# Optimization experiments

Measured on AMD Instinct MI355X. Metric: run time of the kernel, lower is better.

The kernel has to match this reference:

```python
import jax, jax.numpy as jnp
import numpy as np

B, L, D, H, P = 8, 1024, 128, 128, 8
W = 2 * L  # total words
FT = 0.1   # forget-gate floor


def _lin_init(k, out_d, in_d):
    k1, k2 = jax.random.split(k)
    s = 1.0 / np.sqrt(in_d)
    Wm = jax.random.uniform(k1, (out_d, in_d), minval=-s, maxval=s, dtype=jnp.float32)
    b = jax.random.uniform(k2, (out_d,), minval=-s, maxval=s, dtype=jnp.float32)
    return Wm, b


def setup_inputs() -> dict:
    key = jax.random.key(0)
    ks = jax.random.split(key, 32)
    inp = {
        "word_span0": jax.random.normal(ks[0], (B, L, D), dtype=jnp.float32),
        "word_span1": jax.random.normal(ks[1], (B, L, D), dtype=jnp.float32),
        "node_hidden": jax.random.normal(ks[2], (B, D), dtype=jnp.float32),
        "op_embedding": jax.random.normal(ks[3], (B, P, D), dtype=jnp.float32),
        "word_exist_sequence": jax.random.uniform(ks[4], (B, W), dtype=jnp.float32),
        "word_exist_matrix": jax.random.uniform(ks[5], (B, W, W), dtype=jnp.float32),
        "word_operator": jax.random.uniform(ks[6], (B, W, P), dtype=jnp.float32),
        "word_word": jax.random.uniform(ks[7], (B, W, W), dtype=jnp.float32),
        "depend0": jax.random.uniform(ks[8], (B, L, L), dtype=jnp.float32),
        "depend1": jax.random.uniform(ks[9], (B, L, L), dtype=jnp.float32),
        "goal_word": jax.random.uniform(ks[10], (B, W), dtype=jnp.float32),
    }
    dims = [("w_w_s", H, D), ("w_w_k", H, D), ("w_update", D, 3 * H),
            ("g_w", H, D), ("w_o", D, D), ("b2u_forget", D, 3 * H + D),
            ("b2u_forget2", D, 2 * D), ("linear_output", D, D),
            ("o_w", H, D), ("w_g", D, D), ("u2b_forget", D, 2 * D),
            ("w_o_forget", P, D + P * D), ("w_o_rel", P, D + P * D),
            ("w_o_update", P, 2 * P)]
    for i, (nm, o, ii) in enumerate(dims):
        Wm, b = _lin_init(ks[11 + i], o, ii)
        inp[nm + "_W"] = Wm
        inp[nm + "_b"] = b
    return inp


def _lin(x, Wm, b):
    return x @ Wm.T + b


def _nrm(m):
    # row-normalize by count of nonzero entries (torch normalize_matrix)
    return m / ((m != 0).sum(-1, keepdims=True).astype(m.dtype) + 1e-30)


def _l2(x):
    return x / (jnp.linalg.norm(x, axis=-1, keepdims=True) + 1e-30)


def _hgcn(span0, span1, node_hidden, op_emb, wes, wem, w_op, ww, dep0, dep1, gw, p):
    # ---- Bottom2Up ----
    all_word = jnp.concatenate([span0, span1], axis=1)              # [B,W,D]
    goal_trans = _lin(node_hidden, p["g_w_W"], p["g_w_b"])[:, None, :]  # [B,1,H]
    word_g = _l2(goal_trans * gw[..., None])                        # [B,W,H]
    wk_trans = _lin(all_word, p["w_w_k_W"], p["w_w_k_b"])           # [B,W,H]
    word_w_k = _l2(_nrm(ww * wem) @ wk_trans)                       # [B,W,H]
    word_w_s = _l2(jnp.concatenate(
        [_nrm(dep0) @ _lin(span0, p["w_w_s_W"], p["w_w_s_b"]),
         _nrm(dep1) @ _lin(span1, p["w_w_s_W"], p["w_w_s_b"])], axis=1))
    neighbor = jnp.concatenate([word_g, word_w_k, word_w_s], axis=-1)  # [B,W,3H]
    forget = jax.nn.sigmoid(_lin(jnp.concatenate([all_word, word_g, word_w_k, word_w_s], axis=-1),
                                 p["b2u_forget_W"], p["b2u_forget_b"]))
    word_updated = jnp.clip(forget, FT) * all_word + (1 - forget) * jax.nn.relu(
        _lin(neighbor, p["w_update_W"], p["w_update_b"]))           # [B,W,D]
    word_op = _nrm(jnp.swapaxes(wes[..., None] * w_op, 1, 2)) @ _lin(
        word_updated, p["w_o_W"], p["w_o_b"])                       # [B,P,D]
    forget2 = jax.nn.sigmoid(_lin(jnp.concatenate([op_emb, word_op], axis=-1),
                                  p["b2u_forget2_W"], p["b2u_forget2_b"]))
    op_emb = jnp.clip(forget2, FT) * op_emb + (1 - forget2) * jax.nn.relu(
        _lin(word_op, p["linear_output_W"], p["linear_output_b"]))  # [B,P,D]

    # ---- update_graph ----
    awe_n = _l2(word_updated)
    op_n = _l2(op_emb).reshape(op_emb.shape[0], -1)                 # [B,P*D]
    concate = jnp.concatenate(
        [awe_n, jnp.broadcast_to(op_n[:, None, :], (awe_n.shape[0], awe_n.shape[1], op_n.shape[-1]))],
        axis=-1)                                                    # [B,W,D+P*D]
    fg = jnp.clip(jax.nn.sigmoid(_lin(concate, p["w_o_forget_W"], p["w_o_forget_b"])), FT)
    upd = jax.nn.softmax(jax.nn.relu(_lin(
        jnp.concatenate([w_op, _lin(concate, p["w_o_rel_W"], p["w_o_rel_b"])], axis=-1),
        p["w_o_update_W"], p["w_o_update_b"])), axis=-1)
    w_op_new = fg * w_op + (1 - fg) * upd                           # [B,W,P]

    # ---- Up2Bottom ----
    span0u, span1u = word_updated[:, :L], word_updated[:, L:]
    word_o = _l2(w_op_new @ _lin(op_emb, p["o_w_W"], p["o_w_b"]))   # [B,W,H]
    word_w_k2 = _l2(_nrm(ww * wem) @ _lin(word_updated, p["w_w_k_W"], p["w_w_k_b"]))
    word_w_s2 = _l2(jnp.concatenate(
        [_nrm(dep0) @ _lin(span0u, p["w_w_s_W"], p["w_w_s_b"]),
         _nrm(dep1) @ _lin(span1u, p["w_w_s_W"], p["w_w_s_b"])], axis=1))
    neighbor2 = jnp.concatenate([word_o, word_w_k2, word_w_s2], axis=-1)
    word_updated2 = jax.nn.relu(_lin(neighbor2, p["w_update_W"], p["w_update_b"]))  # [B,W,D]
    goal_w = jnp.einsum('bw,bwd->bd', _nrm(gw * wes), word_updated2)  # [B,D]
    goal_updated = jax.nn.relu(_lin(goal_w, p["w_g_W"], p["w_g_b"]))
    fg3 = jax.nn.sigmoid(_lin(jnp.concatenate([goal_w, node_hidden], axis=-1),
                              p["u2b_forget_W"], p["u2b_forget_b"]))
    goal_next = jnp.clip(fg3, FT) * node_hidden + (1 - fg3) * goal_updated
    return (span0u, span1u, op_emb, goal_next)


def reference(word_span0, word_span1, node_hidden, op_embedding, word_exist_sequence,
              word_exist_matrix, word_operator, word_word, depend0, depend1, goal_word,
              w_w_s_W, w_w_s_b, w_w_k_W, w_w_k_b, w_update_W, w_update_b,
              g_w_W, g_w_b, w_o_W, w_o_b, b2u_forget_W, b2u_forget_b,
              b2u_forget2_W, b2u_forget2_b, linear_output_W, linear_output_b,
              o_w_W, o_w_b, w_g_W, w_g_b, u2b_forget_W, u2b_forget_b,
              w_o_forget_W, w_o_forget_b, w_o_rel_W, w_o_rel_b, w_o_update_W, w_o_update_b):
    p = dict(w_w_s_W=w_w_s_W, w_w_s_b=w_w_s_b, w_w_k_W=w_w_k_W, w_w_k_b=w_w_k_b,
             w_update_W=w_update_W, w_update_b=w_update_b, g_w_W=g_w_W, g_w_b=g_w_b,
             w_o_W=w_o_W, w_o_b=w_o_b, b2u_forget_W=b2u_forget_W, b2u_forget_b=b2u_forget_b,
             b2u_forget2_W=b2u_forget2_W, b2u_forget2_b=b2u_forget2_b,
             linear_output_W=linear_output_W, linear_output_b=linear_output_b,
             o_w_W=o_w_W, o_w_b=o_w_b, w_g_W=w_g_W, w_g_b=w_g_b,
             u2b_forget_W=u2b_forget_W, u2b_forget_b=u2b_forget_b,
             w_o_forget_W=w_o_forget_W, w_o_forget_b=w_o_forget_b,
             w_o_rel_W=w_o_rel_W, w_o_rel_b=w_o_rel_b,
             w_o_update_W=w_o_update_W, w_o_update_b=w_o_update_b)
    return _hgcn(word_span0, word_span1, node_hidden, op_embedding, word_exist_sequence,
                 word_exist_matrix, word_operator, word_word, depend0, depend1, goal_word, p)
```

## Files before the change

kernel.cpp:

```cpp
#include <hip/hip_runtime.h>

constexpr int Bn = 8, Ln = 1024, Dn = 128, Pn = 8, Wn = 2048;
constexpr float FTc = 0.1f;
constexpr int BLDc = Bn * Ln * Dn;
constexpr int BWDc = Bn * Wn * Dn;
constexpr int IDM = 1 << 28;

struct __align__(16) F4 { float v[4]; };

typedef __attribute__((ext_vector_type(8))) __bf16 bf16x8;
typedef __attribute__((ext_vector_type(8))) short short8v;
typedef __attribute__((ext_vector_type(4))) short short4v;
typedef __attribute__((ext_vector_type(4))) float f32x4;

static __device__ __forceinline__ float sigm(float x) { return 1.f / (1.f + expf(-x)); }

static __device__ __forceinline__ short f2bf(float f) {
    unsigned u = __builtin_bit_cast(unsigned, f);
    unsigned r = (u + 0x7FFFu + ((u >> 16) & 1u)) >> 16;
    return (short)r;
}

template<int NSRC, int ACT, int OUT, int BM>
__global__ __launch_bounds__(256)
// ... 75 lines not shown
            if constexpr (ACT == 2) v = sigm(v);
            if constexpr (ACT == 3) {
                float f = fbuf[(size_t)row * 128 + col];
                float base = bbuf[(size_t)row * 128 + col];
                v = fmaxf(f, FTc) * base + (1.f - f) * fmaxf(v, 0.f);
            }
            vals[nf][r] = v;
            if constexpr (OUT & 1) Y[(size_t)row * 128 + col] = v;
            if constexpr (OUT & 2) Yh[(size_t)row * 128 + col] = f2bf(v);
        }
    }
    if constexpr (OUT & 4) {
        short* sS = sW;
        __syncthreads();
        #pragma unroll
        for (int nf = 0; nf < NF; ++nf) {
            int col = cg * CPW + nf * 16 + l15;
            #pragma unroll
            for (int r = 0; r < 4; ++r)
                sS[col * 40 + r0 + r] = f2bf(vals[nf][r]);
        }
        __syncthreads();
        const int bb = outRow0 >> 11, kbo = (outRow0 & 2047) >> 5;
        short* __restrict__ dst = Xblk + ((size_t)(bb * 64 + kbo)) * 4096;
        #pragma unroll
        for (int it = 0; it < 2; ++it) {
            int t2 = tid + it * 256;
            int col = t2 >> 2, k8 = (t2 & 3) * 8;
            *(short8v*)(dst + (size_t)t2 * 8) = *(const short8v*)&sS[col * 40 + k8];
        }
    }
}

template<int AMODE, int WR, bool WRA>
__global__ __launch_bounds__(256)
void mfma_gemm(const float* __restrict__ A0, const float* __restrict__ A1,
               const short* __restrict__ Abf, short* __restrict__ Awr,
               const short* __restrict__ Xblk, short* __restrict__ Yh,
               int NI, int KJ, int xkb0, int ybs, int yoff)
{
    constexpr int BM = WR * 16;
    constexpr int WC = 4 / WR;
    constexpr int NF = 8 / WC;
    constexpr int CPW = 128 / WC;
    __shared__ short sA[BM * 72];
    __shared__ short sB[128 * 72];
    __shared__ float srow[WC][BM];

    const int tid = threadIdx.x;
    const int wave = tid >> 6, lane = tid & 63;
    const int l15 = lane & 15, l4 = lane >> 4;
    const int rg = (WR == 2) ? (wave & 1) : 0;
    const int cg = (WR == 2) ? (wave >> 1) : wave;
    const int b = blockIdx.y;
    const int i0 = blockIdx.x * BM;
    const size_t aBase = ((size_t)b * NI + i0) * KJ;
    const int nkb = KJ >> 6;

    const int arow = tid >> 3, ak8 = (tid & 3) * 8, ak16 = (tid & 7) * 8;

    f32x4 acc[NF];
    #pragma unroll
    for (int nf = 0; nf < NF; ++nf) acc[nf] = (f32x4){0.f, 0.f, 0.f, 0.f};

    short8v ra;
    F4 rav0, rav1, raw0, raw1;
    short8v rb0, rb1, rb2, rb3;

#define LOADA(KB)                                                              \
    if (tid < BM * 8) {                                                        \
        if constexpr (AMODE == 2) {                                            \
            ra = *(const short8v*)(Abf + aBase + (size_t)arow * KJ + (KB)*64 + ak16); \
        } else {                                                               \
            const float* pa = A0 + aBase + (size_t)arow * KJ + (KB)*64 + ak16; \
            rav0 = *(const F4*)pa; rav1 = *(const F4*)(pa + 4);                \
            if constexpr (AMODE == 1) {                                        \
                const float* pb = A1 + aBase + (size_t)arow * KJ + (KB)*64 + ak16; \
                raw0 = *(const F4*)pb; raw1 = *(const F4*)(pb + 4);            \
            }                                                                  \
        }                                                                      \
    }
#define STOREA(KB)                                                             \
    if (tid < BM * 8) {                                                        \
        short8v sv;                                                            \
        if constexpr (AMODE == 2) { sv = ra; }                                 \
        else {                                                                 \
            _Pragma("unroll")                                                  \
            for (int e = 0; e < 4; ++e) {                                      \
                float f0 = rav0.v[e], f1 = rav1.v[e];                          \
                if constexpr (AMODE == 1) { f0 *= raw0.v[e]; f1 *= raw1.v[e]; }\
                sv[e] = f2bf(f0); sv[4 + e] = f2bf(f1);                        \
            }                                                                  \
        }                                                                      \
        *(short8v*)&sA[arow * 72 + ak16] = sv;                                 \
        if constexpr (WRA)                                                     \
            *(short8v*)(Awr + aBase + (size_t)arow * KJ + (KB)*64 + ak16) = sv;\
    }
#define LOADB(KB)                                                              \
    {                                                                          \
        const short* s0 = Xblk + ((size_t)(b * 64 + xkb0 + (KB)*2)) * 4096;    \
        rb0 = *(const short8v*)(s0 + (size_t)tid * 8);                         \
        rb1 = *(const short8v*)(s0 + (size_t)(tid + 256) * 8);                 \
        rb2 = *(const short8v*)(s0 + 4096 + (size_t)tid * 8);                  \
        rb3 = *(const short8v*)(s0 + 4096 + (size_t)(tid + 256) * 8);          \
    }
#define STOREB()                                                               \
    {                                                                          \
        int c0 = tid >> 2;            int c1 = (tid + 256) >> 2;               \
        *(short8v*)&sB[c0 * 72 + ak8]      = rb0;                              \
        *(short8v*)&sB[c1 * 72 + ak8]      = rb1;                              \
        *(short8v*)&sB[c0 * 72 + 32 + ak8] = rb2;                              \
        *(short8v*)&sB[c1 * 72 + 32 + ak8] = rb3;                              \
    }

    LOADA(0); LOADB(0);
    STOREA(0); STOREB();
    __syncthreads();

    for (int kb = 0; kb < nkb; ++kb) {
        const bool more = (kb + 1 < nkb);
        if (more) { LOADA(kb + 1); LOADB(kb + 1); }
        #pragma unroll
        for (int ksub = 0; ksub < 2; ++ksub) {
            bf16x8 af = *(const bf16x8*)&sA[(rg * 16 + l15) * 72 + ksub * 32 + l4 * 8];
            #pragma unroll
            for (int nf = 0; nf < NF; ++nf) {
                bf16x8 bv = *(const bf16x8*)&sB[(cg * CPW + nf * 16 + l15) * 72 + ksub * 32 + l4 * 8];
                acc[nf] = __builtin_amdgcn_mfma_f32_16x16x32_bf16(af, bv, acc[nf], 0, 0, 0);
            }
        }
        if (more) {
            __syncthreads();
            STOREA(kb + 1); STOREB();
            __syncthreads();
        }
    }
#undef LOADA
#undef STOREA
#undef LOADB
#undef STOREB

    float s[4];
    #pragma unroll
    for (int r = 0; r < 4; ++r) {
        float t = 0.f;
        #pragma unroll
        for (int nf = 0; nf < NF; ++nf) t += acc[nf][r] * acc[nf][r];
        t += __shfl_xor(t, 1); t += __shfl_xor(t, 2);
        t += __shfl_xor(t, 4); t += __shfl_xor(t, 8);
        s[r] = t;
    }
    __syncthreads();
    if (l15 == 0) {
        #pragma unroll
        for (int r = 0; r < 4; ++r) srow[cg][rg * 16 + l4 * 4 + r] = s[r];
    }
    __syncthreads();
    const int rbase = b * ybs + yoff + i0 + rg * 16 + l4 * 4;
    #pragma unroll
    for (int r = 0; r < 4; ++r) {
        float tot = 0.f;
        #pragma unroll
        for (int c = 0; c < WC; ++c) tot += srow[c][rg * 16 + l4 * 4 + r];
        float inv = 1.f / (sqrtf(tot) + 1e-30f);
        #pragma unroll
        for (int nf = 0; nf < NF; ++nf)
            Yh[(size_t)(rbase + r) * 128 + cg * CPW + nf * 16 + l15] = f2bf(acc[nf][r] * inv);
    }
}

__global__ void k_allword(const float* __restrict__ s0, const float* __restrict__ s1,
                          float* __restrict__ aw, short* __restrict__ awh)
{
    int i = blockIdx.x * 256 + threadIdx.x;
    int b = i / (Ln * Dn / 4);
    F4 v0 = ((const F4*)s0)[i];
    F4 v1 = ((const F4*)s1)[i];
    int d0 = i + b * (Ln * Dn / 4);
    int d1 = i + (b + 1) * (Ln * Dn / 4);
    ((F4*)aw)[d0] = v0;
    ((F4*)aw)[d1] = v1;
    short4v h0, h1;
    #pragma unroll
    for (int e = 0; e < 4; ++e) { h0[e] = f2bf(v0.v[e]); h1[e] = f2bf(v1.v[e]); }
    ((short4v*)awh)[d0] = h0;
    ((short4v*)awh)[d1] = h1;
}

__global__ void k_goalg(const float* __restrict__ node, const float* __restrict__ Wg,
                        const float* __restrict__ bg, float* __restrict__ gvec,
                        float* __restrict__ gnorm)
{
    int b = blockIdx.x, h = threadIdx.x;
    float s = bg[h];
    for (int k = 0; k < 128; ++k) s += node[b * 128 + k] * Wg[h * 128 + k];
    gvec[b * 128 + h] = s;
    __shared__ float red[128];
    red[h] = s * s; __syncthreads();
    for (int st = 64; st > 0; st >>= 1) { if (h < st) red[h] += red[h + st]; __syncthreads(); }
    if (h == 0) gnorm[b] = sqrtf(red[0]);
}
// ... 288 lines not shown
    float* out = (float*)d_out;
    float* out_op   = out + 2 * BLDc;
    float* out_goal = out + 2 * BLDc + Bn * Pn * Dn;

    float* ws = (float*)d_ws;
    float* allword = ws;
    float* wupd    = ws + 1 * BWDc;
    float* tmpA    = ws + 2 * BWDc;
    float* tmpB    = ws + 3 * BWDc;
    float* sm      = ws + 4 * BWDc;
    float* gvec   = sm;
    float* gnorm  = sm + 1024;
    float* wordop = sm + 1056;
    float* opembN = sm + 9248;
    float* opn    = sm + 17440;
    float* cf     = sm + 25632;
    float* crel   = sm + 25696;
    float* opw    = sm + 25760;
    float* goalw  = sm + 33952;
    float* fgb    = sm + 34976;
    float* relb   = sm + 166048;
    float* wopn   = sm + 297120;

    short* allwordh = (short*)(ws + 4 * (size_t)BWDc + 458752);
    short* wupdh  = allwordh + BWDc;
    short* wordgh = wupdh + BWDc;
    short* wwkh   = wordgh + BWDc;
    short* wwsh   = wwkh + BWDc;
    short* Xblk   = wwsh + BWDc;
    short* Awwem  = Xblk + BWDc;
    short* dep0b  = Awwem + (size_t)Bn * Wn * Wn;
    short* dep1b  = dep0b + (size_t)Bn * Ln * Ln;

    const dim3 blk(256);

    k_allword<<<1024, blk, 0, stream>>>(span0, span1, allword, allwordh);
    linmfma<1,0,4,32><<<512, blk, 0, stream>>>(allwordh, nullptr, nullptr, nullptr,
        wwk_W, wwk_b, nullptr, nullptr, Xblk, IDM, 0, 0, IDM, 0, 0, nullptr, nullptr);
    mfma_gemm<1,2,true><<<dim3(64, 8), blk, 0, stream>>>(ww, wem, nullptr, Awwem,
        Xblk, wwkh, Wn, Wn, 0, Wn, 0);
    linmfma<1,0,4,32><<<256, blk, 0, stream>>>(allwordh, nullptr, nullptr, nullptr,
        wws_W, wws_b, nullptr, nullptr, Xblk, Ln, Wn, 0, Ln, Wn, 0, nullptr, nullptr);
    linmfma<1,0,4,32><<<256, blk, 0, stream>>>(allwordh, nullptr, nullptr, nullptr,
        wws_W, wws_b, nullptr, nullptr, Xblk, Ln, Wn, Ln, Ln, Wn, Ln, nullptr, nullptr);
    mfma_gemm<0,1,true><<<dim3(64, 8), blk, 0, stream>>>(dep0, nullptr, nullptr, dep0b,
        Xblk, wwsh, Ln, Ln, 0, Wn, 0);
    mfma_gemm<0,1,true><<<dim3(64, 8), blk, 0, stream>>>(dep1, nullptr, nullptr, dep1b,
        Xblk, wwsh, Ln, Ln, 32, Wn, Ln);
    k_goalg<<<8, 128, 0, stream>>>(node, gw_W, gw_b, gvec, gnorm);
    k_wordg<<<16384, 128, 0, stream>>>(gvec, gnorm, gw, wordgh);
    linmfma<4,2,1,16><<<1024, blk, 0, stream>>>(allwordh, wordgh, wwkh, wwsh,
        bf_W, bf_b, tmpB, nullptr, nullptr, IDM, 0, 0, IDM, 0, 0, nullptr, nullptr);
    linmfma<3,3,3,16><<<1024, blk, 0, stream>>>(wordgh, wwkh, wwsh, nullptr,
        wup_W, wup_b, wupd, wupdh, nullptr, IDM, 0, 0, IDM, 0, 0, tmpB, allword);
    linmfma<1,0,1,16><<<1024, blk, 0, stream>>>(wupdh, nullptr, nullptr, nullptr,
        wo_W, wo_b, tmpA, nullptr, nullptr, IDM, 0, 0, IDM, 0, 0, nullptr, nullptr);
    k_wordop_part<<<dim3(64, 8), blk, 0, stream>>>(wes, wopr, tmpA, tmpB, tmpB + 524288);
    k_wordop_fin<<<64, 128, 0, stream>>>(tmpB, tmpB + 524288, wordop);
    k_opemb<<<64, 128, 0, stream>>>(opemb, wordop, bf2_W, bf2_b, lo_W, lo_b, opembN, out_op);
    k_opn<<<64, 128, 0, stream>>>(opembN, opn);
    k_cfrel<<<64, blk, 0, stream>>>(opn, wof_W, wof_b, wor_W, wor_b, cf, crel);
    k_fgrel<<<512, blk, 0, stream>>>(wupd, wof_W, wor_W, cf, crel, fgb, relb);
    k_wopnew<<<64, blk, 0, stream>>>(wopr, fgb, relb, wou_W, wou_b, wopn);
    k_opw<<<64, 128, 0, stream>>>(opembN, ow_W, ow_b, opw);
    k_wordo<<<16384, 128, 0, stream>>>(wopn, opw, wordgh);

    linmfma<1,0,4,32><<<512, blk, 0, stream>>>(wupdh, nullptr, nullptr, nullptr,
        wwk_W, wwk_b, nullptr, nullptr, Xblk, IDM, 0, 0, IDM, 0, 0, nullptr, nullptr);
    mfma_gemm<2,2,false><<<dim3(64, 8), blk, 0, stream>>>(nullptr, nullptr, Awwem, nullptr,
        Xblk, wwkh, Wn, Wn, 0, Wn, 0);
    linmfma<1,0,4,32><<<256, blk, 0, stream>>>(wupdh, nullptr, nullptr, nullptr,
        wws_W, wws_b, nullptr, nullptr, Xblk, Ln, Wn, 0, Ln, Wn, 0, nullptr, nullptr);
    linmfma<1,0,4,32><<<256, blk, 0, stream>>>(wupdh, nullptr, nullptr, nullptr,
        wws_W, wws_b, nullptr, nullptr, Xblk, Ln, Wn, Ln, Ln, Wn, Ln, nullptr, nullptr);
    mfma_gemm<2,1,false><<<dim3(64, 8), blk, 0, stream>>>(nullptr, nullptr, dep0b, nullptr,
        Xblk, wwsh, Ln, Ln, 0, Wn, 0);
    mfma_gemm<2,1,false><<<dim3(64, 8), blk, 0, stream>>>(nullptr, nullptr, dep1b, nullptr,
        Xblk, wwsh, Ln, Ln, 32, Wn, Ln);
    linmfma<3,1,1,16><<<1024, blk, 0, stream>>>(wordgh, wwkh, wwsh, nullptr,
        wup_W, wup_b, tmpA, nullptr, nullptr, IDM, 0, 0, IDM, 0, 0, nullptr, nullptr);
    k_goalw_part<<<dim3(64, 8), blk, 0, stream>>>(gw, wes, tmpA, tmpB, tmpB + 65536);
    k_goalw_fin<<<8, 128, 0, stream>>>(tmpB, tmpB + 65536, goalw);
    k_goalnext<<<8, 128, 0, stream>>>(goalw, node, wg_W, wg_b, u2b_W, u2b_b, out_goal);
    k_copyspans<<<2048, blk, 0, stream>>>(wupd, out);
}
```

Before: 375.4 us.

## Split K across two wave groups in adjacency GEMM with LDS reduction

The row-normalized adjacency GEMM kernel now runs 512 threads per block, and each group of four waves processes one half of the K dimension using its own shared-memory A/B buffers. At the end, the second group writes its partial accumulators to shared memory and the first group adds them before the row norm and bf16 store. The goal is more waves in flight per block and a shorter serial K loop, which helps hide global-load latency in these memory-bound GEMMs. In exchange it doubles LDS use and adds an extra reduction step with barriers.

```diff
diff --git a/kernel.cpp b/kernel.cpp
--- a/kernel.cpp
+++ b/kernel.cpp
@@ -131,32 +131,39 @@
     }
 }
 
-template<int AMODE, int WR, bool WRA>
-__global__ __launch_bounds__(256)
-void mfma_gemm(const float* __restrict__ A0, const float* __restrict__ A1,
-               const short* __restrict__ Abf, short* __restrict__ Awr,
-               const short* __restrict__ Xblk, short* __restrict__ Yh,
-               int NI, int KJ, int xkb0, int ybs, int yoff)
-{
-    constexpr int BM = WR * 16;
+template<int AMODE, int BM, bool WRA>
+__global__ __launch_bounds__(512)
+void mfma_gemm2(const float* __restrict__ A0, const float* __restrict__ A1,
+                const short* __restrict__ Abf, short* __restrict__ Awr,
+                const short* __restrict__ Xblk, short* __restrict__ Yh,
+                int NI, int KJ, int xkb0, int ybs, int yoff)
+{
+    constexpr int WR = BM / 16;
     constexpr int WC = 4 / WR;
     constexpr int NF = 8 / WC;
     constexpr int CPW = 128 / WC;
-    __shared__ short sA[BM * 72];
-    __shared__ short sB[128 * 72];
+    __shared__ short sA[2][BM * 72];
+    __shared__ short sB[2][128 * 72];
     __shared__ float srow[WC][BM];
 
     const int tid = threadIdx.x;
     const int wave = tid >> 6, lane = tid & 63;
     const int l15 = lane & 15, l4 = lane >> 4;
-    const int rg = (WR == 2) ? (wave & 1) : 0;
-    const int cg = (WR == 2) ? (wave >> 1) : wave;
+    const int kg = wave >> 2;
+    const int sub = wave & 3;
+    const int rg = (WR == 2) ? (sub >> 1) : 0;
+    const int cg = (WR == 2) ? (sub & 1) : sub;
+    const int half = tid >> 8;
+    const int th = tid & 255;
     const int b = blockIdx.y;
     const int i0 = blockIdx.x * BM;
     const size_t aBase = ((size_t)b * NI + i0) * KJ;
-    const int nkb = KJ >> 6;
-
-    const int arow = tid >> 3, ak8 = (tid & 3) * 8, ak16 = (tid & 7) * 8;
+    const int KH = KJ >> 1;
+    const int nkb = KH >> 6;
+    const int kofs = half * KH;
+    const int cbase = b * 64 + xkb0 + half * (KH >> 5);
+
+    const int arow = th >> 3, ak16 = (th & 7) * 8, ak8 = (th & 3) * 8;
 
     f32x4 acc[NF];
     #pragma unroll
@@ -167,20 +174,19 @@
     short8v rb0, rb1, rb2, rb3;
 
 #define LOADA(KB)                                                              \
-    if (tid < BM * 8) {                                                        \
+    if (th < BM * 8) {                                                         \
+        size_t aoff = aBase + (size_t)arow * KJ + kofs + (KB)*64 + ak16;       \
         if constexpr (AMODE == 2) {                                            \
-            ra = *(const short8v*)(Abf + aBase + (size_t)arow * KJ + (KB)*64 + ak16); \
+            ra = *(const short8v*)(Abf + aoff);                                \
         } else {                                                               \
-            const float* pa = A0 + aBase + (size_t)arow * KJ + (KB)*64 + ak16; \
-            rav0 = *(const F4*)pa; rav1 = *(const F4*)(pa + 4);                \
+            rav0 = *(const F4*)(A0 + aoff); rav1 = *(const F4*)(A0 + aoff + 4);\
             if constexpr (AMODE == 1) {                                        \
-                const float* pb = A1 + aBase + (size_t)arow * KJ + (KB)*64 + ak16; \
-                raw0 = *(const F4*)pb; raw1 = *(const F4*)(pb + 4);            \
+                raw0 = *(const F4*)(A1 + aoff); raw1 = *(const F4*)(A1 + aoff + 4); \
             }                                                                  \
         }                                                                      \
     }
 #define STOREA(KB)                                                             \
-    if (tid < BM * 8) {                                                        \
+    if (th < BM * 8) {                                                         \
         short8v sv;                                                            \
         if constexpr (AMODE == 2) { sv = ra; }                                 \
         else {                                                                 \
@@ -191,25 +197,25 @@
                 sv[e] = f2bf(f0); sv[4 + e] = f2bf(f1);                        \
             }                                                                  \
         }                                                                      \
-        *(short8v*)&sA[arow * 72 + ak16] = sv;                                 \
+        *(short8v*)&sA[half][arow * 72 + ak16] = sv;                           \
         if constexpr (WRA)                                                     \
-            *(short8v*)(Awr + aBase + (size_t)arow * KJ + (KB)*64 + ak16) = sv;\
+            *(short8v*)(Awr + aBase + (size_t)arow * KJ + kofs + (KB)*64 + ak16) = sv; \
     }
 #define LOADB(KB)                                                              \
     {                                                                          \
-        const short* s0 = Xblk + ((size_t)(b * 64 + xkb0 + (KB)*2)) * 4096;    \
-        rb0 = *(const short8v*)(s0 + (size_t)tid * 8);                         \
-        rb1 = *(const short8v*)(s0 + (size_t)(tid + 256) * 8);                 \
-        rb2 = *(const short8v*)(s0 + 4096 + (size_t)tid * 8);                  \
-        rb3 = *(const short8v*)(s0 + 4096 + (size_t)(tid + 256) * 8);          \
+        const short* s0 = Xblk + ((size_t)(cbase + (KB)*2)) * 4096;            \
+        rb0 = *(const short8v*)(s0 + (size_t)th * 8);                          \
+        rb1 = *(const short8v*)(s0 + (size_t)(th + 256) * 8);                  \
+        rb2 = *(const short8v*)(s0 + 4096 + (size_t)th * 8);                   \
+        rb3 = *(const short8v*)(s0 + 4096 + (size_t)(th + 256) * 8);           \
     }
 #define STOREB()                                                               \
     {                                                                          \
-        int c0 = tid >> 2;            int c1 = (tid + 256) >> 2;               \
-        *(short8v*)&sB[c0 * 72 + ak8]      = rb0;                              \
-        *(short8v*)&sB[c1 * 72 + ak8]      = rb1;                              \
-        *(short8v*)&sB[c0 * 72 + 32 + ak8] = rb2;                              \
-        *(short8v*)&sB[c1 * 72 + 32 + ak8] = rb3;                              \
+        int c0 = th >> 2;             int c1 = (th + 256) >> 2;                \
+        *(short8v*)&sB[half][c0 * 72 + ak8]      = rb0;                        \
+        *(short8v*)&sB[half][c1 * 72 + ak8]      = rb1;                        \
+        *(short8v*)&sB[half][c0 * 72 + 32 + ak8] = rb2;                        \
+        *(short8v*)&sB[half][c1 * 72 + 32 + ak8] = rb3;                        \
     }
 
     LOADA(0); LOADB(0);
@@ -221,10 +227,10 @@
         if (more) { LOADA(kb + 1); LOADB(kb + 1); }
         #pragma unroll
         for (int ksub = 0; ksub < 2; ++ksub) {
-            bf16x8 af = *(const bf16x8*)&sA[(rg * 16 + l15) * 72 + ksub * 32 + l4 * 8];
+            bf16x8 af = *(const bf16x8*)&sA[kg][(rg * 16 + l15) * 72 + ksub * 32 + l4 * 8];
             #pragma unroll
             for (int nf = 0; nf < NF; ++nf) {
-                bf16x8 bv = *(const bf16x8*)&sB[(cg * CPW + nf * 16 + l15) * 72 + ksub * 32 + l4 * 8];
+                bf16x8 bv = *(const bf16x8*)&sB[kg][(cg * CPW + nf * 16 + l15) * 72 + ksub * 32 + l4 * 8];
                 acc[nf] = __builtin_amdgcn_mfma_f32_16x16x32_bf16(af, bv, acc[nf], 0, 0, 0);
             }
         }
@@ -239,32 +245,50 @@
 #undef LOADB
 #undef STOREB
 
+    float* sC = (float*)&sB[0][0];
+    __syncthreads();
+    if (kg == 1) {
+        #pragma unroll
+        for (int nf = 0; nf < NF; ++nf)
+            #pragma unroll
+            for (int r = 0; r < 4; ++r)
+                sC[(rg * 16 + l4 * 4 + r) * 132 + cg * CPW + nf * 16 + l15] = acc[nf][r];
+    }
+    __syncthreads();
     float s[4];
-    #pragma unroll
-    for (int r = 0; r < 4; ++r) {
-        float t = 0.f;
-        #pragma unroll
-        for (int nf = 0; nf < NF; ++nf) t += acc[nf][r] * acc[nf][r];
-        t += __shfl_xor(t, 1); t += __shfl_xor(t, 2);
-        t += __shfl_xor(t, 4); t += __shfl_xor(t, 8);
-        s[r] = t;
-    }
-    __syncthreads();
-    if (l15 == 0) {
-        #pragma unroll
-        for (int r = 0; r < 4; ++r) srow[cg][rg * 16 + l4 * 4 + r] = s[r];
-    }
-    __syncthreads();
-    const int rbase = b * ybs + yoff + i0 + rg * 16 + l4 * 4;
-    #pragma unroll
-    for (int r = 0; r < 4; ++r) {
-        float tot = 0.f;
-        #pragma unroll
-        for (int c = 0; c < WC; ++c) tot += srow[c][rg * 16 + l4 * 4 + r];
-        float inv = 1.f / (sqrtf(tot) + 1e-30f);
+    if (kg == 0) {
         #pragma unroll
         for (int nf = 0; nf < NF; ++nf)
-            Yh[(size_t)(rbase + r) * 128 + cg * CPW + nf * 16 + l15] = f2bf(acc[nf][r] * inv);
+            #pragma unroll
+            for (int r = 0; r < 4; ++r)
+                acc[nf][r] += sC[(rg * 16 + l4 * 4 + r) * 132 + cg * CPW + nf * 16 + l15];
+        #pragma unroll
+        for (int r = 0; r < 4; ++r) {
+            float t = 0.f;
+            #pragma unroll
+            for (int nf = 0; nf < NF; ++nf) t += acc[nf][r] * acc[nf][r];
+            t += __shfl_xor(t, 1); t += __shfl_xor(t, 2);
+            t += __shfl_xor(t, 4); t += __shfl_xor(t, 8);
+            s[r] = t;
+        }
+        if (l15 == 0) {
+            #pragma unroll
+            for (int r = 0; r < 4; ++r) srow[cg][rg * 16 + l4 * 4 + r] = s[r];
+        }
+    }
+    __syncthreads();
+    if (kg == 0) {
+        const int rbase = b * ybs + yoff + i0 + rg * 16 + l4 * 4;
+        #pragma unroll
+        for (int r = 0; r < 4; ++r) {
+            float tot = 0.f;
+            #pragma unroll
+            for (int c = 0; c < WC; ++c) tot += srow[c][rg * 16 + l4 * 4 + r];
+            float inv = 1.f / (sqrtf(tot) + 1e-30f);
+            #pragma unroll
+            for (int nf = 0; nf < NF; ++nf)
+                Yh[(size_t)(rbase + r) * 128 + cg * CPW + nf * 16 + l15] = f2bf(acc[nf][r] * inv);
+        }
     }
 }
 
@@ -621,19 +645,20 @@
     short* dep1b  = dep0b + (size_t)Bn * Ln * Ln;
 
     const dim3 blk(256);
+    const dim3 blk512(512);
 
     k_allword<<<1024, blk, 0, stream>>>(span0, span1, allword, allwordh);
     linmfma<1,0,4,32><<<512, blk, 0, stream>>>(allwordh, nullptr, nullptr, nullptr,
         wwk_W, wwk_b, nullptr, nullptr, Xblk, IDM, 0, 0, IDM, 0, 0, nullptr, nullptr);
-    mfma_gemm<1,2,true><<<dim3(64, 8), blk, 0, stream>>>(ww, wem, nullptr, Awwem,
+    mfma_gemm2<1,32,true><<<dim3(64, 8), blk512, 0, stream>>>(ww, wem, nullptr, Awwem,
         Xblk, wwkh, Wn, Wn, 0, Wn, 0);
     linmfma<1,0,4,32><<<256, blk, 0, stream>>>(allwordh, nullptr, nullptr, nullptr,
         wws_W, wws_b, nullptr, nullptr, Xblk, Ln, Wn, 0, Ln, Wn, 0, nullptr, nullptr);
     linmfma<1,0,4,32><<<256, blk, 0, stream>>>(allwordh, nullptr, nullptr, nullptr,
         wws_W, wws_b, nullptr, nullptr, Xblk, Ln, Wn, Ln, Ln, Wn, Ln, nullptr, nullptr);
-    mfma_gemm<0,1,true><<<dim3(64, 8), blk, 0, stream>>>(dep0, nullptr, nullptr, dep0b,
+    mfma_gemm2<0,16,true><<<dim3(64, 8), blk512, 0, stream>>>(dep0, nullptr, nullptr, dep0b,
         Xblk, wwsh, Ln, Ln, 0, Wn, 0);
-    mfma_gemm<0,1,true><<<dim3(64, 8), blk, 0, stream>>>(dep1, nullptr, nullptr, dep1b,
+    mfma_gemm2<0,16,true><<<dim3(64, 8), blk512, 0, stream>>>(dep1, nullptr, nullptr, dep1b,
         Xblk, wwsh, Ln, Ln, 32, Wn, Ln);
     k_goalg<<<8, 128, 0, stream>>>(node, gw_W, gw_b, gvec, gnorm);
     k_wordg<<<16384, 128, 0, stream>>>(gvec, gnorm, gw, wordgh);
@@ -655,15 +680,15 @@
 
     linmfma<1,0,4,32><<<512, blk, 0, stream>>>(wupdh, nullptr, nullptr, nullptr,
         wwk_W, wwk_b, nullptr, nullptr, Xblk, IDM, 0, 0, IDM, 0, 0, nullptr, nullptr);
-    mfma_gemm<2,2,false><<<dim3(64, 8), blk, 0, stream>>>(nullptr, nullptr, Awwem, nullptr,
+    mfma_gemm2<2,32,false><<<dim3(64, 8), blk512, 0, stream>>>(nullptr, nullptr, Awwem, nullptr,
         Xblk, wwkh, Wn, Wn, 0, Wn, 0);
     linmfma<1,0,4,32><<<256, blk, 0, stream>>>(wupdh, nullptr, nullptr, nullptr,
         wws_W, wws_b, nullptr, nullptr, Xblk, Ln, Wn, 0, Ln, Wn, 0, nullptr, nullptr);
     linmfma<1,0,4,32><<<256, blk, 0, stream>>>(wupdh, nullptr, nullptr, nullptr,
         wws_W, wws_b, nullptr, nullptr, Xblk, Ln, Wn, Ln, Ln, Wn, Ln, nullptr, nullptr);
-    mfma_gemm<2,1,false><<<dim3(64, 8), blk, 0, stream>>>(nullptr, nullptr, dep0b, nullptr,
+    mfma_gemm2<2,16,false><<<dim3(64, 8), blk512, 0, stream>>>(nullptr, nullptr, dep0b, nullptr,
         Xblk, wwsh, Ln, Ln, 0, Wn, 0);
-    mfma_gemm<2,1,false><<<dim3(64, 8), blk, 0, stream>>>(nullptr, nullptr, dep1b, nullptr,
+    mfma_gemm2<2,16,false><<<dim3(64, 8), blk512, 0, stream>>>(nullptr, nullptr, dep1b, nullptr,
         Xblk, wwsh, Ln, Ln, 32, Wn, Ln);
     linmfma<3,1,1,16><<<1024, blk, 0, stream>>>(wordgh, wwkh, wwsh, nullptr,
         wup_W, wup_b, tmpA, nullptr, nullptr, IDM, 0, 0, IDM, 0, 0, nullptr, nullptr);
```

Result: faster. 356.8 us (-5.0%).

## Replace LDS-staged adjacency GEMM with register-direct MFMA operand loads

Applied to the files above, without the earlier changes.

The shared-memory-staged GEMM for the adjacency products is replaced by a 128-thread kernel in which each wave owns 16 rows and all 128 output columns. The wave loads its A fragments and the pre-blocked B operand straight from global memory into MFMA registers, so the LDS buffers and barriers go away. Each row's L2 norm is now computed within one wave without a cross-wave reduction. In exchange, B fragments are re-read from global or L2 by every wave instead of being shared through LDS, A loads are narrower per lane, and there is no explicit prefetch pipeline.

```diff
diff --git a/kernel.cpp b/kernel.cpp
--- a/kernel.cpp
+++ b/kernel.cpp
@@ -131,141 +131,75 @@
     }
 }
 
-template<int AMODE, int WR, bool WRA>
-__global__ __launch_bounds__(256)
-void mfma_gemm(const float* __restrict__ A0, const float* __restrict__ A1,
-               const short* __restrict__ Abf, short* __restrict__ Awr,
-               const short* __restrict__ Xblk, short* __restrict__ Yh,
-               int NI, int KJ, int xkb0, int ybs, int yoff)
-{
-    constexpr int BM = WR * 16;
-    constexpr int WC = 4 / WR;
-    constexpr int NF = 8 / WC;
-    constexpr int CPW = 128 / WC;
-    __shared__ short sA[BM * 72];
-    __shared__ short sB[128 * 72];
-    __shared__ float srow[WC][BM];
-
+template<int AMODE, bool WRA>
+__global__ __launch_bounds__(128)
+void mfma_gemm3(const float* __restrict__ A0, const float* __restrict__ A1,
+                const short* __restrict__ Abf, short* __restrict__ Awr,
+                const short* __restrict__ Xblk, short* __restrict__ Yh,
+                int NI, int KJ, int xkb0, int ybs, int yoff)
+{
     const int tid = threadIdx.x;
     const int wave = tid >> 6, lane = tid & 63;
     const int l15 = lane & 15, l4 = lane >> 4;
-    const int rg = (WR == 2) ? (wave & 1) : 0;
-    const int cg = (WR == 2) ? (wave >> 1) : wave;
     const int b = blockIdx.y;
-    const int i0 = blockIdx.x * BM;
-    const size_t aBase = ((size_t)b * NI + i0) * KJ;
+    const int i0 = blockIdx.x * 32 + wave * 16;
+    const size_t aRow = ((size_t)b * NI + i0 + l15) * KJ;
     const int nkb = KJ >> 6;
-
-    const int arow = tid >> 3, ak8 = (tid & 3) * 8, ak16 = (tid & 7) * 8;
-
-    f32x4 acc[NF];
-    #pragma unroll
-    for (int nf = 0; nf < NF; ++nf) acc[nf] = (f32x4){0.f, 0.f, 0.f, 0.f};
-
-    short8v ra;
-    F4 rav0, rav1, raw0, raw1;
-    short8v rb0, rb1, rb2, rb3;
-
-#define LOADA(KB)                                                              \
-    if (tid < BM * 8) {                                                        \
-        if constexpr (AMODE == 2) {                                            \
-            ra = *(const short8v*)(Abf + aBase + (size_t)arow * KJ + (KB)*64 + ak16); \
-        } else {                                                               \
-            const float* pa = A0 + aBase + (size_t)arow * KJ + (KB)*64 + ak16; \
-            rav0 = *(const F4*)pa; rav1 = *(const F4*)(pa + 4);                \
-            if constexpr (AMODE == 1) {                                        \
-                const float* pb = A1 + aBase + (size_t)arow * KJ + (KB)*64 + ak16; \
-                raw0 = *(const F4*)pb; raw1 = *(const F4*)(pb + 4);            \
-            }                                                                  \
-        }                                                                      \
-    }
-#define STOREA(KB)                                                             \
-    if (tid < BM * 8) {                                                        \
-        short8v sv;                                                            \
-        if constexpr (AMODE == 2) { sv = ra; }                                 \
-        else {                                                                 \
-            _Pragma("unroll")                                                  \
-            for (int e = 0; e < 4; ++e) {                                      \
-                float f0 = rav0.v[e], f1 = rav1.v[e];                          \
-                if constexpr (AMODE == 1) { f0 *= raw0.v[e]; f1 *= raw1.v[e]; }\
-                sv[e] = f2bf(f0); sv[4 + e] = f2bf(f1);                        \
-            }                                                                  \
-        }                                                                      \
-        *(short8v*)&sA[arow * 72 + ak16] = sv;                                 \
-        if constexpr (WRA)                                                     \
-            *(short8v*)(Awr + aBase + (size_t)arow * KJ + (KB)*64 + ak16) = sv;\
-    }
-#define LOADB(KB)                                                              \
-    {                                                                          \
-        const short* s0 = Xblk + ((size_t)(b * 64 + xkb0 + (KB)*2)) * 4096;    \
-        rb0 = *(const short8v*)(s0 + (size_t)tid * 8);                         \
-        rb1 = *(const short8v*)(s0 + (size_t)(tid + 256) * 8);                 \
-        rb2 = *(const short8v*)(s0 + 4096 + (size_t)tid * 8);                  \
-        rb3 = *(const short8v*)(s0 + 4096 + (size_t)(tid + 256) * 8);          \
-    }
-#define STOREB()                                                               \
-    {                                                                          \
-        int c0 = tid >> 2;            int c1 = (tid + 256) >> 2;               \
-        *(short8v*)&sB[c0 * 72 + ak8]      = rb0;                              \
-        *(short8v*)&sB[c1 * 72 + ak8]      = rb1;                              \
-        *(short8v*)&sB[c0 * 72 + 32 + ak8] = rb2;                              \
-        *(short8v*)&sB[c1 * 72 + 32 + ak8] = rb3;                              \
-    }
-
-    LOADA(0); LOADB(0);
-    STOREA(0); STOREB();
-    __syncthreads();
-
+    const int cb0 = b * 64 + xkb0;
+    const int lko = l4 * 8;
+
+    f32x4 acc[8];
+    #pragma unroll
+    for (int nf = 0; nf < 8; ++nf) acc[nf] = (f32x4){0.f, 0.f, 0.f, 0.f};
+
+    #pragma unroll 2
     for (int kb = 0; kb < nkb; ++kb) {
-        const bool more = (kb + 1 < nkb);
-        if (more) { LOADA(kb + 1); LOADB(kb + 1); }
         #pragma unroll
         for (int ksub = 0; ksub < 2; ++ksub) {
-            bf16x8 af = *(const bf16x8*)&sA[(rg * 16 + l15) * 72 + ksub * 32 + l4 * 8];
+            const int ko = kb * 64 + ksub * 32 + lko;
+            bf16x8 af;
+            if constexpr (AMODE == 2) {
+                af = *(const bf16x8*)(Abf + aRow + ko);
+            } else {
+                F4 v0 = *(const F4*)(A0 + aRow + ko);
+                F4 v1 = *(const F4*)(A0 + aRow + ko + 4);
+                if constexpr (AMODE == 1) {
+                    F4 w0 = *(const F4*)(A1 + aRow + ko);
+                    F4 w1 = *(const F4*)(A1 + aRow + ko + 4);
+                    #pragma unroll
+                    for (int e = 0; e < 4; ++e) { v0.v[e] *= w0.v[e]; v1.v[e] *= w1.v[e]; }
+                }
+                short8v sv;
+                #pragma unroll
+                for (int e = 0; e < 4; ++e) { sv[e] = f2bf(v0.v[e]); sv[4 + e] = f2bf(v1.v[e]); }
+                if constexpr (WRA) *(short8v*)(Awr + aRow + ko) = sv;
+                af = __builtin_bit_cast(bf16x8, sv);
+            }
+            const short* bp = Xblk + ((size_t)(cb0 + kb * 2 + ksub)) * 4096 + lko;
             #pragma unroll
-            for (int nf = 0; nf < NF; ++nf) {
-                bf16x8 bv = *(const bf16x8*)&sB[(cg * CPW + nf * 16 + l15) * 72 + ksub * 32 + l4 * 8];
+            for (int nf = 0; nf < 8; ++nf) {
+                bf16x8 bv = *(const bf16x8*)(bp + (nf * 16 + l15) * 32);
                 acc[nf] = __builtin_amdgcn_mfma_f32_16x16x32_bf16(af, bv, acc[nf], 0, 0, 0);
             }
         }
-        if (more) {
-            __syncthreads();
-            STOREA(kb + 1); STOREB();
-            __syncthreads();
-        }
-    }
-#undef LOADA
-#undef STOREA
-#undef LOADB
-#undef STOREB
-
-    float s[4];
+    }
+
+    float inv[4];
     #pragma unroll
     for (int r = 0; r < 4; ++r) {
         float t = 0.f;
         #pragma unroll
-        for (int nf = 0; nf < NF; ++nf) t += acc[nf][r] * acc[nf][r];
+        for (int nf = 0; nf < 8; ++nf) t += acc[nf][r] * acc[nf][r];
         t += __shfl_xor(t, 1); t += __shfl_xor(t, 2);
         t += __shfl_xor(t, 4); t += __shfl_xor(t, 8);
-        s[r] = t;
-    }
-    __syncthreads();
-    if (l15 == 0) {
-        #pragma unroll
-        for (int r = 0; r < 4; ++r) srow[cg][rg * 16 + l4 * 4 + r] = s[r];
-    }
-    __syncthreads();
-    const int rbase = b * ybs + yoff + i0 + rg * 16 + l4 * 4;
-    #pragma unroll
-    for (int r = 0; r < 4; ++r) {
-        float tot = 0.f;
-        #pragma unroll
-        for (int c = 0; c < WC; ++c) tot += srow[c][rg * 16 + l4 * 4 + r];
-        float inv = 1.f / (sqrtf(tot) + 1e-30f);
-        #pragma unroll
-        for (int nf = 0; nf < NF; ++nf)
-            Yh[(size_t)(rbase + r) * 128 + cg * CPW + nf * 16 + l15] = f2bf(acc[nf][r] * inv);
-    }
+        inv[r] = 1.f / (sqrtf(t) + 1e-30f);
+    }
+    const int rbase = b * ybs + yoff + i0 + l4 * 4;
+    #pragma unroll
+    for (int nf = 0; nf < 8; ++nf)
+        #pragma unroll
+        for (int r = 0; r < 4; ++r)
+            Yh[(size_t)(rbase + r) * 128 + nf * 16 + l15] = f2bf(acc[nf][r] * inv[r]);
 }
 
 __global__ void k_allword(const float* __restrict__ s0, const float* __restrict__ s1,
@@ -621,19 +555,20 @@
     short* dep1b  = dep0b + (size_t)Bn * Ln * Ln;
 
     const dim3 blk(256);
+    const dim3 blk128(128);
 
     k_allword<<<1024, blk, 0, stream>>>(span0, span1, allword, allwordh);
     linmfma<1,0,4,32><<<512, blk, 0, stream>>>(allwordh, nullptr, nullptr, nullptr,
         wwk_W, wwk_b, nullptr, nullptr, Xblk, IDM, 0, 0, IDM, 0, 0, nullptr, nullptr);
-    mfma_gemm<1,2,true><<<dim3(64, 8), blk, 0, stream>>>(ww, wem, nullptr, Awwem,
+    mfma_gemm3<1,true><<<dim3(64, 8), blk128, 0, stream>>>(ww, wem, nullptr, Awwem,
         Xblk, wwkh, Wn, Wn, 0, Wn, 0);
     linmfma<1,0,4,32><<<256, blk, 0, stream>>>(allwordh, nullptr, nullptr, nullptr,
         wws_W, wws_b, nullptr, nullptr, Xblk, Ln, Wn, 0, Ln, Wn, 0, nullptr, nullptr);
     linmfma<1,0,4,32><<<256, blk, 0, stream>>>(allwordh, nullptr, nullptr, nullptr,
         wws_W, wws_b, nullptr, nullptr, Xblk, Ln, Wn, Ln, Ln, Wn, Ln, nullptr, nullptr);
-    mfma_gemm<0,1,true><<<dim3(64, 8), blk, 0, stream>>>(dep0, nullptr, nullptr, dep0b,
+    mfma_gemm3<0,true><<<dim3(32, 8), blk128, 0, stream>>>(dep0, nullptr, nullptr, dep0b,
         Xblk, wwsh, Ln, Ln, 0, Wn, 0);
-    mfma_gemm<0,1,true><<<dim3(64, 8), blk, 0, stream>>>(dep1, nullptr, nullptr, dep1b,
+    mfma_gemm3<0,true><<<dim3(32, 8), blk128, 0, stream>>>(dep1, nullptr, nullptr, dep1b,
         Xblk, wwsh, Ln, Ln, 32, Wn, Ln);
     k_goalg<<<8, 128, 0, stream>>>(node, gw_W, gw_b, gvec, gnorm);
     k_wordg<<<16384, 128, 0, stream>>>(gvec, gnorm, gw, wordgh);
@@ -655,15 +590,15 @@
 
     linmfma<1,0,4,32><<<512, blk, 0, stream>>>(wupdh, nullptr, nullptr, nullptr,
         wwk_W, wwk_b, nullptr, nullptr, Xblk, IDM, 0, 0, IDM, 0, 0, nullptr, nullptr);
-    mfma_gemm<2,2,false><<<dim3(64, 8), blk, 0, stream>>>(nullptr, nullptr, Awwem, nullptr,
+    mfma_gemm3<2,false><<<dim3(64, 8), blk128, 0, stream>>>(nullptr, nullptr, Awwem, nullptr,
         Xblk, wwkh, Wn, Wn, 0, Wn, 0);
     linmfma<1,0,4,32><<<256, blk, 0, stream>>>(wupdh, nullptr, nullptr, nullptr,
         wws_W, wws_b, nullptr, nullptr, Xblk, Ln, Wn, 0, Ln, Wn, 0, nullptr, nullptr);
     linmfma<1,0,4,32><<<256, blk, 0, stream>>>(wupdh, nullptr, nullptr, nullptr,
         wws_W, wws_b, nullptr, nullptr, Xblk, Ln, Wn, Ln, Ln, Wn, Ln, nullptr, nullptr);
-    mfma_gemm<2,1,false><<<dim3(64, 8), blk, 0, stream>>>(nullptr, nullptr, dep0b, nullptr,
+    mfma_gemm3<2,false><<<dim3(32, 8), blk128, 0, stream>>>(nullptr, nullptr, dep0b, nullptr,
         Xblk, wwsh, Ln, Ln, 0, Wn, 0);
-    mfma_gemm<2,1,false><<<dim3(64, 8), blk, 0, stream>>>(nullptr, nullptr, dep1b, nullptr,
+    mfma_gemm3<2,false><<<dim3(32, 8), blk128, 0, stream>>>(nullptr, nullptr, dep1b, nullptr,
         Xblk, wwsh, Ln, Ln, 32, Wn, Ln);
     linmfma<3,1,1,16><<<1024, blk, 0, stream>>>(wordgh, wwkh, wwsh, nullptr,
         wup_W, wup_b, tmpA, nullptr, nullptr, IDM, 0, 0, IDM, 0, 0, nullptr, nullptr);
```

Result: slower. 734.3 us (+95.6%).

## Split-K the big adjacency GEMMs with fp32 partials and a separate normalize pass

Applied to the files above, without the earlier changes.

Replaces the monolithic adjacency GEMM kernel, which fused the L2 row normalization, with a split-K variant. Each K chunk writes fp32 partial sums to scratch buffers, and a new finalize kernel adds the partials, L2-normalizes each row and writes bf16. This raises the block count from 512 to up to 2048 so more CUs stay busy, and fixes the row tile at 32. The cost is extra kernel launches, fp32 partial traffic through global memory, and reuse of existing scratch buffers (dep0b, tmpA, tmpB) as partial storage, which risks aliasing.

```diff
diff --git a/kernel.cpp b/kernel.cpp
--- a/kernel.cpp
+++ b/kernel.cpp
@@ -131,56 +131,48 @@
     }
 }
 
-template<int AMODE, int WR, bool WRA>
+template<int AMODE, bool WRA>
 __global__ __launch_bounds__(256)
-void mfma_gemm(const float* __restrict__ A0, const float* __restrict__ A1,
+void mfma_part(const float* __restrict__ A0, const float* __restrict__ A1,
                const short* __restrict__ Abf, short* __restrict__ Awr,
-               const short* __restrict__ Xblk, short* __restrict__ Yh,
-               int NI, int KJ, int xkb0, int ybs, int yoff)
-{
-    constexpr int BM = WR * 16;
-    constexpr int WC = 4 / WR;
-    constexpr int NF = 8 / WC;
-    constexpr int CPW = 128 / WC;
-    __shared__ short sA[BM * 72];
+               const short* __restrict__ Xblk, float* __restrict__ part,
+               int NI, int KJ, int KL, int xkb0)
+{
+    __shared__ short sA[32 * 72];
     __shared__ short sB[128 * 72];
-    __shared__ float srow[WC][BM];
-
     const int tid = threadIdx.x;
     const int wave = tid >> 6, lane = tid & 63;
     const int l15 = lane & 15, l4 = lane >> 4;
-    const int rg = (WR == 2) ? (wave & 1) : 0;
-    const int cg = (WR == 2) ? (wave >> 1) : wave;
-    const int b = blockIdx.y;
-    const int i0 = blockIdx.x * BM;
-    const size_t aBase = ((size_t)b * NI + i0) * KJ;
-    const int nkb = KJ >> 6;
-
-    const int arow = tid >> 3, ak8 = (tid & 3) * 8, ak16 = (tid & 7) * 8;
-
-    f32x4 acc[NF];
-    #pragma unroll
-    for (int nf = 0; nf < NF; ++nf) acc[nf] = (f32x4){0.f, 0.f, 0.f, 0.f};
+    const int rg = wave >> 1, cg = wave & 1;
+    const int b = blockIdx.y, kc = blockIdx.z;
+    const int i0 = blockIdx.x * 32;
+    const size_t aBase = ((size_t)b * NI + i0) * KJ + (size_t)kc * KL;
+    const int nkb = KL >> 6;
+    const int cbase = b * 64 + xkb0 + ((kc * KL) >> 5);
+    const int arow = tid >> 3, ak16 = (tid & 7) * 8, ak8 = (tid & 3) * 8;
+
+    f32x4 acc[4];
+    #pragma unroll
+    for (int nf = 0; nf < 4; ++nf) acc[nf] = (f32x4){0.f, 0.f, 0.f, 0.f};
 
     short8v ra;
     F4 rav0, rav1, raw0, raw1;
     short8v rb0, rb1, rb2, rb3;
 
 #define LOADA(KB)                                                              \
-    if (tid < BM * 8) {                                                        \
+    {                                                                          \
+        size_t aoff = aBase + (size_t)arow * KJ + (KB)*64 + ak16;              \
         if constexpr (AMODE == 2) {                                            \
-            ra = *(const short8v*)(Abf + aBase + (size_t)arow * KJ + (KB)*64 + ak16); \
+            ra = *(const short8v*)(Abf + aoff);                                \
         } else {                                                               \
-            const float* pa = A0 + aBase + (size_t)arow * KJ + (KB)*64 + ak16; \
-            rav0 = *(const F4*)pa; rav1 = *(const F4*)(pa + 4);                \
+            rav0 = *(const F4*)(A0 + aoff); rav1 = *(const F4*)(A0 + aoff + 4);\
             if constexpr (AMODE == 1) {                                        \
-                const float* pb = A1 + aBase + (size_t)arow * KJ + (KB)*64 + ak16; \
-                raw0 = *(const F4*)pb; raw1 = *(const F4*)(pb + 4);            \
+                raw0 = *(const F4*)(A1 + aoff); raw1 = *(const F4*)(A1 + aoff + 4); \
             }                                                                  \
         }                                                                      \
     }
 #define STOREA(KB)                                                             \
-    if (tid < BM * 8) {                                                        \
+    {                                                                          \
         short8v sv;                                                            \
         if constexpr (AMODE == 2) { sv = ra; }                                 \
         else {                                                                 \
@@ -197,7 +189,7 @@
     }
 #define LOADB(KB)                                                              \
     {                                                                          \
-        const short* s0 = Xblk + ((size_t)(b * 64 + xkb0 + (KB)*2)) * 4096;    \
+        const short* s0 = Xblk + ((size_t)(cbase + (KB)*2)) * 4096;            \
         rb0 = *(const short8v*)(s0 + (size_t)tid * 8);                         \
         rb1 = *(const short8v*)(s0 + (size_t)(tid + 256) * 8);                 \
         rb2 = *(const short8v*)(s0 + 4096 + (size_t)tid * 8);                  \
@@ -223,8 +215,8 @@
         for (int ksub = 0; ksub < 2; ++ksub) {
             bf16x8 af = *(const bf16x8*)&sA[(rg * 16 + l15) * 72 + ksub * 32 + l4 * 8];
             #pragma unroll
-            for (int nf = 0; nf < NF; ++nf) {
-                bf16x8 bv = *(const bf16x8*)&sB[(cg * CPW + nf * 16 + l15) * 72 + ksub * 32 + l4 * 8];
+            for (int nf = 0; nf < 4; ++nf) {
+                bf16x8 bv = *(const bf16x8*)&sB[(cg * 64 + nf * 16 + l15) * 72 + ksub * 32 + l4 * 8];
                 acc[nf] = __builtin_amdgcn_mfma_f32_16x16x32_bf16(af, bv, acc[nf], 0, 0, 0);
             }
         }
@@ -239,33 +231,26 @@
 #undef LOADB
 #undef STOREB
 
-    float s[4];
-    #pragma unroll
-    for (int r = 0; r < 4; ++r) {
-        float t = 0.f;
-        #pragma unroll
-        for (int nf = 0; nf < NF; ++nf) t += acc[nf][r] * acc[nf][r];
-        t += __shfl_xor(t, 1); t += __shfl_xor(t, 2);
-        t += __shfl_xor(t, 4); t += __shfl_xor(t, 8);
-        s[r] = t;
-    }
-    __syncthreads();
-    if (l15 == 0) {
-        #pragma unroll
-        for (int r = 0; r < 4; ++r) srow[cg][rg * 16 + l4 * 4 + r] = s[r];
-    }
-    __syncthreads();
-    const int rbase = b * ybs + yoff + i0 + rg * 16 + l4 * 4;
-    #pragma unroll
-    for (int r = 0; r < 4; ++r) {
-        float tot = 0.f;
-        #pragma unroll
-        for (int c = 0; c < WC; ++c) tot += srow[c][rg * 16 + l4 * 4 + r];
-        float inv = 1.f / (sqrtf(tot) + 1e-30f);
-        #pragma unroll
-        for (int nf = 0; nf < NF; ++nf)
-            Yh[(size_t)(rbase + r) * 128 + cg * CPW + nf * 16 + l15] = f2bf(acc[nf][r] * inv);
-    }
+    const size_t pbase = (((size_t)kc * Bn + b) * NI + i0 + rg * 16 + l4 * 4) * 128 + cg * 64;
+    #pragma unroll
+    for (int nf = 0; nf < 4; ++nf)
+        #pragma unroll
+        for (int r = 0; r < 4; ++r)
+            part[pbase + (size_t)r * 128 + nf * 16 + l15] = acc[nf][r];
+}
+
+__global__ void k_gemm_fin(const float* __restrict__ part, short* __restrict__ Yh,
+                           int NI, int KCH, int ybs, int yoff)
+{
+    int row = blockIdx.x; int b = row / NI; int i = row - b * NI;
+    int h = threadIdx.x;
+    float s = 0.f;
+    for (int kc = 0; kc < KCH; ++kc)
+        s += part[(((size_t)kc * Bn + b) * NI + i) * 128 + h];
+    __shared__ float red[128];
+    red[h] = s * s; __syncthreads();
+    for (int st = 64; st > 0; st >>= 1) { if (h < st) red[h] += red[h + st]; __syncthreads(); }
+    Yh[(size_t)(b * ybs + yoff + i) * 128 + h] = f2bf(s / (sqrtf(red[0]) + 1e-30f));
 }
 
 __global__ void k_allword(const float* __restrict__ s0, const float* __restrict__ s1,
@@ -620,21 +605,29 @@
     short* dep0b  = Awwem + (size_t)Bn * Wn * Wn;
     short* dep1b  = dep0b + (size_t)Bn * Ln * Ln;
 
+    float* partWW1 = (float*)dep0b;
+    float* partWW2 = tmpA;
+    float* partD0  = tmpA;
+    float* partD1  = tmpB;
+
     const dim3 blk(256);
 
     k_allword<<<1024, blk, 0, stream>>>(span0, span1, allword, allwordh);
     linmfma<1,0,4,32><<<512, blk, 0, stream>>>(allwordh, nullptr, nullptr, nullptr,
         wwk_W, wwk_b, nullptr, nullptr, Xblk, IDM, 0, 0, IDM, 0, 0, nullptr, nullptr);
-    mfma_gemm<1,2,true><<<dim3(64, 8), blk, 0, stream>>>(ww, wem, nullptr, Awwem,
-        Xblk, wwkh, Wn, Wn, 0, Wn, 0);
+    mfma_part<1,true><<<dim3(64, 8, 4), blk, 0, stream>>>(ww, wem, nullptr, Awwem,
+        Xblk, partWW1, Wn, Wn, 512, 0);
+    k_gemm_fin<<<16384, 128, 0, stream>>>(partWW1, wwkh, Wn, 4, Wn, 0);
     linmfma<1,0,4,32><<<256, blk, 0, stream>>>(allwordh, nullptr, nullptr, nullptr,
         wws_W, wws_b, nullptr, nullptr, Xblk, Ln, Wn, 0, Ln, Wn, 0, nullptr, nullptr);
     linmfma<1,0,4,32><<<256, blk, 0, stream>>>(allwordh, nullptr, nullptr, nullptr,
         wws_W, wws_b, nullptr, nullptr, Xblk, Ln, Wn, Ln, Ln, Wn, Ln, nullptr, nullptr);
-    mfma_gemm<0,1,true><<<dim3(64, 8), blk, 0, stream>>>(dep0, nullptr, nullptr, dep0b,
-        Xblk, wwsh, Ln, Ln, 0, Wn, 0);
-    mfma_gemm<0,1,true><<<dim3(64, 8), blk, 0, stream>>>(dep1, nullptr, nullptr, dep1b,
-        Xblk, wwsh, Ln, Ln, 32, Wn, Ln);
+    mfma_part<0,true><<<dim3(32, 8, 2), blk, 0, stream>>>(dep0, nullptr, nullptr, dep0b,
+        Xblk, partD0, Ln, Ln, 512, 0);
+    k_gemm_fin<<<8192, 128, 0, stream>>>(partD0, wwsh, Ln, 2, Wn, 0);
+    mfma_part<0,true><<<dim3(32, 8, 2), blk, 0, stream>>>(dep1, nullptr, nullptr, dep1b,
+        Xblk, partD1, Ln, Ln, 512, 32);
+    k_gemm_fin<<<8192, 128, 0, stream>>>(partD1, wwsh, Ln, 2, Wn, Ln);
     k_goalg<<<8, 128, 0, stream>>>(node, gw_W, gw_b, gvec, gnorm);
     k_wordg<<<16384, 128, 0, stream>>>(gvec, gnorm, gw, wordgh);
     linmfma<4,2,1,16><<<1024, blk, 0, stream>>>(allwordh, wordgh, wwkh, wwsh,
@@ -655,16 +648,19 @@
 
     linmfma<1,0,4,32><<<512, blk, 0, stream>>>(wupdh, nullptr, nullptr, nullptr,
         wwk_W, wwk_b, nullptr, nullptr, Xblk, IDM, 0, 0, IDM, 0, 0, nullptr, nullptr);
-    mfma_gemm<2,2,false><<<dim3(64, 8), blk, 0, stream>>>(nullptr, nullptr, Awwem, nullptr,
-        Xblk, wwkh, Wn, Wn, 0, Wn, 0);
+    mfma_part<2,false><<<dim3(64, 8, 2), blk, 0, stream>>>(nullptr, nullptr, Awwem, nullptr,
+        Xblk, partWW2, Wn, Wn, 1024, 0);
+    k_gemm_fin<<<16384, 128, 0, stream>>>(partWW2, wwkh, Wn, 2, Wn, 0);
     linmfma<1,0,4,32><<<256, blk, 0, stream>>>(wupdh, nullptr, nullptr, nullptr,
         wws_W, wws_b, nullptr, nullptr, Xblk, Ln, Wn, 0, Ln, Wn, 0, nullptr, nullptr);
     linmfma<1,0,4,32><<<256, blk, 0, stream>>>(wupdh, nullptr, nullptr, nullptr,
         wws_W, wws_b, nullptr, nullptr, Xblk, Ln, Wn, Ln, Ln, Wn, Ln, nullptr, nullptr);
-    mfma_gemm<2,1,false><<<dim3(64, 8), blk, 0, stream>>>(nullptr, nullptr, dep0b, nullptr,
-        Xblk, wwsh, Ln, Ln, 0, Wn, 0);
-    mfma_gemm<2,1,false><<<dim3(64, 8), blk, 0, stream>>>(nullptr, nullptr, dep1b, nullptr,
-        Xblk, wwsh, Ln, Ln, 32, Wn, Ln);
+    mfma_part<2,false><<<dim3(32, 8, 2), blk, 0, stream>>>(nullptr, nullptr, dep0b, nullptr,
+        Xblk, partD0, Ln, Ln, 512, 0);
+    k_gemm_fin<<<8192, 128, 0, stream>>>(partD0, wwsh, Ln, 2, Wn, 0);
+    mfma_part<2,false><<<dim3(32, 8, 2), blk, 0, stream>>>(nullptr, nullptr, dep1b, nullptr,
+        Xblk, partD1, Ln, Ln, 512, 32);
+    k_gemm_fin<<<8192, 128, 0, stream>>>(partD1, wwsh, Ln, 2, Wn, Ln);
     linmfma<3,1,1,16><<<1024, blk, 0, stream>>>(wordgh, wwkh, wwsh, nullptr,
         wup_W, wup_b, tmpA, nullptr, nullptr, IDM, 0, 0, IDM, 0, 0, nullptr, nullptr);
     k_goalw_part<<<dim3(64, 8), blk, 0, stream>>>(gw, wes, tmpA, tmpB, tmpB + 65536);
```

Result: slower. 410.4 us (+9.3%).
